# Kernel optimization log

Hardware: AMD Instinct MI355X
Metric: run time of the kernel (lower is better)

The kernel has to match this reference:

```python
import jax, jax.numpy as jnp
import numpy as np

QMAX = 127.0  # int8 symmetric
EPS = 1e-8

def _quant_dequant(v, axis):
    # symmetric int8 fake-quant along `axis` (per-row for weights, per-token for acts)
    scale = jnp.max(jnp.abs(v), axis=axis, keepdims=True) / QMAX
    scale = jnp.maximum(scale, EPS)
    q = jnp.clip(jnp.round(v / scale), -QMAX, QMAX)
    return q * scale

def _ste(v, axis):
    # straight-through estimator: identity gradient through quantization
    return v + jax.lax.stop_gradient(_quant_dequant(v, axis) - v)

def setup_inputs() -> dict:
    key = jax.random.key(0)
    k1, k2, k3 = jax.random.split(key, 3)
    H, I = 2048, 5632
    x = jax.random.normal(k1, (4, 2048, H), dtype=jnp.float32)
    # nn.Linear weight layout: [out_features, in_features]
    w_gate_up = jax.random.normal(k2, (2 * I, H), dtype=jnp.float32) * (H ** -0.5)
    w_down = jax.random.normal(k3, (H, I), dtype=jnp.float32) * (I ** -0.5)
    return {"x": x, "w_gate_up": w_gate_up, "w_down": w_down}

def reference(x, w_gate_up, w_down):
    I = w_down.shape[1]
    # QLinear #1: quantize act per-token, weight per-out-channel, dequant matmul
    xq = _ste(x, axis=-1)                       # [B,S,H]
    w1q = _ste(w_gate_up, axis=-1)              # [2I,H]
    gate_up = jnp.einsum('bsh,oh->bso', xq, w1q)  # [B,S,2I]
    gate, up = gate_up[..., :I], gate_up[..., I:]
    h = jax.nn.silu(gate) * up                  # SwiGLU, [B,S,I]
    # QLinear #2
    hq = _ste(h, axis=-1)
    w2q = _ste(w_down, axis=-1)                 # [H,I]
    return jnp.einsum('bsi,oi->bso', hq, w2q)   # [B,S,H]
```

## Files before the change

kernel.cpp:

```cpp
#include <hip/hip_runtime.h>
#include <hip/hip_bf16.h>
#include <stdint.h>

#define H_DIM 2048
#define I_DIM 5632
#define M_DIM 8192
#define N1_DIM (2 * I_DIM)
#define NBN1 (I_DIM / 128)
#define NPART (NBN1 * 4)
#define QS1 2304
#define QS2 5888

typedef __attribute__((ext_vector_type(4))) int i32x4;

__device__ __forceinline__ void gload16(const void* g, void* l) {
  __builtin_amdgcn_global_load_lds(
      reinterpret_cast<const __attribute__((address_space(1))) uint32_t*>(
          reinterpret_cast<uintptr_t>(g)),
      reinterpret_cast<__attribute__((address_space(3))) uint32_t*>(
          reinterpret_cast<uintptr_t>(l)),
      16, 0, 0);
}

__device__ __forceinline__ i32x4 ds_read128(uint32_t addr) {
  i32x4 d;
  asm volatile("s_mov_b32 m0, -1\n\tds_read_b128 %0, %1"
               : "=v"(d)
               : "v"(addr));
  return d;
}

#define MEMF() asm volatile("" ::: "memory")
#define BAR()                      \
  do {                             \
    MEMF();                        \
    __builtin_amdgcn_s_barrier();  \
    MEMF();                        \
  } while (0)
#define SCHEDB() __builtin_amdgcn_sched_barrier(0)

__global__ __launch_bounds__(256) void quant_rows_f32(
    const float* __restrict__ in, int8_t* __restrict__ q,
    float* __restrict__ scl, int rowlen, int qstride) {
  const int row = blockIdx.x;
  const int tid = threadIdx.x;
  const float* rp = in + (size_t)row * rowlen;
  float m = 0.f;
  for (int i = tid * 4; i < rowlen; i += 1024) {
    const float4 v = *reinterpret_cast<const float4*>(rp + i);
    m = fmaxf(m, fmaxf(fmaxf(fabsf(v.x), fabsf(v.y)),
                       fmaxf(fabsf(v.z), fabsf(v.w))));
  }
#pragma unroll
  for (int o = 32; o; o >>= 1) m = fmaxf(m, __shfl_xor(m, o));
  __shared__ float wm[4];
  if ((tid & 63) == 0) wm[tid >> 6] = m;
  __syncthreads();
  m = fmaxf(fmaxf(wm[0], wm[1]), fmaxf(wm[2], wm[3]));
  const float scale = fmaxf(m / 127.0f, 1e-8f);
  const float inv = 1.0f / scale;
  if (tid == 0) scl[row] = scale;
  int8_t* qp = q + (size_t)row * qstride;
  for (int i = tid * 4; i < rowlen; i += 1024) {
    const float4 v = *reinterpret_cast<const float4*>(rp + i);
    const int a = (int)rintf(fminf(fmaxf(v.x * inv, -127.f), 127.f));
    const int b = (int)rintf(fminf(fmaxf(v.y * inv, -127.f), 127.f));
    const int c = (int)rintf(fminf(fmaxf(v.z * inv, -127.f), 127.f));
    const int d = (int)rintf(fminf(fmaxf(v.w * inv, -127.f), 127.f));
    *reinterpret_cast<int*>(qp + i) =
        (a & 255) | ((b & 255) << 8) | ((c & 255) << 16) | (d << 24);
  }
}

__global__ __launch_bounds__(256) void quant_h_rows(
    const __hip_bfloat16* __restrict__ h, const float* __restrict__ hpart,
    int8_t* __restrict__ q, float* __restrict__ scl) {
  const int row = blockIdx.x;
  const int tid = threadIdx.x;
  float m = (tid < NPART) ? hpart[(size_t)row * NPART + tid] : 0.f;
#pragma unroll
  for (int o = 32; o; o >>= 1) m = fmaxf(m, __shfl_xor(m, o));
  __shared__ float wm[4];
  if ((tid & 63) == 0) wm[tid >> 6] = m;
  __syncthreads();
  m = fmaxf(fmaxf(wm[0], wm[1]), fmaxf(wm[2], wm[3]));
  const float scale = fmaxf(m / 127.0f, 1e-8f);
  const float inv = 1.0f / scale;
  if (tid == 0) scl[row] = scale;
  const __hip_bfloat16* rp = h + (size_t)row * I_DIM;
  int8_t* qp = q + (size_t)row * QS2;
  for (int i = tid * 8; i < I_DIM; i += 2048) {
    const uint4 v = *reinterpret_cast<const uint4*>(rp + i);
    const uint32_t w[4] = {v.x, v.y, v.z, v.w};
    int pk0 = 0, pk1 = 0;
#pragma unroll
    for (int j = 0; j < 8; ++j) {
      const float f =
          __uint_as_float(((w[j >> 1] >> ((j & 1) * 16)) & 0xffffu) << 16);
      const int qv = (int)rintf(fminf(fmaxf(f * inv, -127.f), 127.f));
      if (j < 4) pk0 |= (qv & 255) << ((j & 3) * 8);
      else       pk1 |= (qv & 255) << ((j & 3) * 8);
    }
    *reinterpret_cast<int2*>(qp + i) = make_int2(pk0, pk1);
  }
}

#define RD_A(MH, BUF)                                                          \
  do {                                                                         \
    _Pragma("unroll") for (int m = 0; m < 4; ++m) {                            \
      a[MH][m][0] = ds_read128(aB0 + (BUF) + (MH)*16384 + m * 2048);           \
      a[MH][m][1] = ds_read128(aB1 + (BUF) + (MH)*16384 + m * 2048);           \
    }                                                                          \
  } while (0)

#define RD_B(NH, BUF)                                                          \
  do {                                                                         \
    _Pragma("unroll") for (int n = 0; n < 2; ++n) {                            \
      b[NH][n][0] = ds_read128(bB0 + (BUF) + (NH)*16384 + n * 2048);           \
      b[NH][n][1] = ds_read128(bB1 + (BUF) + (NH)*16384 + n * 2048);           \
    }                                                                          \
  } while (0)

#define MFMA_Q(MH, NH)                                                         \
  do {                                                                         \
    __builtin_amdgcn_s_setprio(1);                                             \
    _Pragma("unroll") for (int kk = 0; kk < 2; ++kk)                           \
        _Pragma("unroll") for (int m = 0; m < 4; ++m)                          \
            _Pragma("unroll") for (int n = 0; n < 2; ++n) acc[MH][m][NH][n] =  \
        __builtin_amdgcn_mfma_i32_16x16x64_i8(a[MH][m][kk], b[NH][n][kk],      \
                                              acc[MH][m][NH][n], 0, 0, 0);     \
    __builtin_amdgcn_s_setprio(0);                                             \
  } while (0)

#define KTILE_BODY(SA, SB)                                                     \
  do {                                                                         \
    const int cb = (t & 1) * 32768;                                            \
    const int nb = cb ^ 32768;                                                 \
                                                                      \
    SCHEDB();                                                                  \
    RD_B(1, cb);                                                               \
    MEMF();                                                                    \
    if (t + 1 < KT) SA(1, t + 1);                                              \
    asm volatile("s_waitcnt lgkmcnt(4)" ::: "memory");                         \
    SCHEDB();                                                                  \
    MFMA_Q(0, 0);                                                              \
    BAR();                                                                     \
                                                                      \
    SCHEDB();                                                                  \
    RD_A(1, cb);                                                               \
    MEMF();                                                                    \
    if (t + 1 < KT) SB(1, t + 1);                                              \
    asm volatile("s_waitcnt lgkmcnt(8)" ::: "memory");                         \
    SCHEDB();                                                                  \
    MFMA_Q(0, 1);                                                              \
    BAR();                                                                     \
                                                                      \
    SCHEDB();                                                                  \
    if (t + 2 < KT) SA(0, t + 2);                                              \
    asm volatile("s_waitcnt lgkmcnt(0)" ::: "memory");                         \
    SCHEDB();                                                                  \
    MFMA_Q(1, 0);                                                              \
    if (t + 2 < KT) asm volatile("s_waitcnt vmcnt(6)" ::: "memory");           \
    else            asm volatile("s_waitcnt vmcnt(0)" ::: "memory");           \
    BAR();                                                                     \
                                                                      \
    SCHEDB();                                                                  \
    if (t + 1 < KT) { RD_A(0, nb); RD_B(0, nb); }                              \
    MEMF();                                                                    \
    if (t + 2 < KT) SB(0, t + 2);                                              \
    MFMA_Q(1, 1);                                                              \
    if (t + 1 < KT) {                                                          \
      if (t + 2 < KT) asm volatile("s_waitcnt vmcnt(4)" ::: "memory");         \
      else            asm volatile("s_waitcnt vmcnt(0)" ::: "memory");         \
    }                                                                          \
    BAR();                                                                     \
  } while (0)

__global__ __launch_bounds__(512, 2) void gemm1_silu(
    const int8_t* __restrict__ qx, const float* __restrict__ sx,
    const int8_t* __restrict__ qw, const float* __restrict__ sw,
    __hip_bfloat16* __restrict__ h, float* __restrict__ hpart) {
  __shared__ int8_t lds[131072];
  const int tid = threadIdx.x;
  const int lane = tid & 63;
  const int wid = tid >> 6;
  const int wr = wid >> 2, wc = wid & 3;
  const int c16 = lane & 15, kq = lane >> 4, r7 = lane & 7, lr = lane >> 3;
  const int sslot = ((lane & 7) ^ lr) << 4;
  const int sl0 = (kq ^ r7) << 4;
  const int sl1 = ((4 + kq) ^ r7) << 4;

  const int id = blockIdx.x;
  const int x = id & 7;
  const int j = id >> 3;
  const int bm = ((x & 1) << 4) + j / 11;
  const int bn = (x >> 1) * 11 + j % 11;

  const int xrow = wid * 8 + lr;
  const int fx = (xrow & ~31) | ((xrow & 15) << 1) | ((xrow >> 4) & 1);

  const size_t goffA = (size_t)(bm * 256 + xrow) * QS1 + sslot;
  const size_t goffG = (size_t)(bn * 128 + fx) * QS1 + sslot;
  const size_t goffU = goffG + (size_t)I_DIM * QS1;
  const int ldsAw = wid * 8 * 128;
  const int ldsBw = 65536 + wid * 8 * 128;

  const uint32_t L = (uint32_t)(uintptr_t)(void*)&lds[0];
  const uint32_t aB0 = L + (wr * 64 + c16) * 128 + sl0;
  const uint32_t aB1 = L + (wr * 64 + c16) * 128 + sl1;
  const uint32_t bB0 = L + 65536 + (wc * 32 + c16) * 128 + sl0;
  const uint32_t bB1 = L + 65536 + (wc * 32 + c16) * 128 + sl1;

  i32x4 acc[2][4][2][2] = {};
  i32x4 a[2][4][2], b[2][2][2];

#define STAGE_A1(half, t)                                                      \
  do {                                                                         \
    const int _b = ((t) & 1) * 32768;                                          \
    _Pragma("unroll") for (int ld = 0; ld < 2; ++ld)                           \
        gload16(qx + goffA + (size_t)((half)*128 + ld * 64) * QS1 +            \
                    (size_t)(t) * 128,                                         \
                lds + _b + ldsAw + ((half)*128 + ld * 64) * 128);              \
  } while (0)

#define STAGE_B1(half, t)                                                      \
  do {                                                                         \
    const int _b = ((t) & 1) * 32768;                                          \
    const int8_t* _s = (half) ? (qw + goffU) : (qw + goffG);                   \
    _Pragma("unroll") for (int ld = 0; ld < 2; ++ld)                           \
        gload16(_s + (size_t)(ld * 64) * QS1 + (size_t)(t) * 128,              \
                lds + _b + ldsBw + ((half)*128 + ld * 64) * 128);              \
  } while (0)

  const int KT = H_DIM / 128;
  STAGE_A1(0, 0); STAGE_B1(0, 0); STAGE_A1(1, 0); STAGE_B1(1, 0);
  STAGE_A1(0, 1); STAGE_B1(0, 1);
  asm volatile("s_waitcnt vmcnt(4)" ::: "memory");
  BAR();
  RD_A(0, 0); RD_B(0, 0);
  MEMF();

#pragma unroll 1
  for (int t = 0; t < KT; ++t) {
    KTILE_BODY(STAGE_A1, STAGE_B1);
  }

  const int row0 = bm * 256 + wr * 64 + kq * 4;
  const int colb = bn * 128 + wc * 32 + 2 * c16;
#pragma unroll
  for (int mh = 0; mh < 2; ++mh) {
#pragma unroll
    for (int m = 0; m < 4; ++m) {
#pragma unroll
      for (int r = 0; r < 4; ++r) {
        const int row = row0 + mh * 128 + m * 16 + r;
        const float sxr = sx[row];
        float hv[2];
#pragma unroll
        for (int n = 0; n < 2; ++n) {
          const int col = colb + n;
          const float g = (float)acc[mh][m][0][n][r] * (sxr * sw[col]);
          const float u = (float)acc[mh][m][1][n][r] * (sxr * sw[I_DIM + col]);
          hv[n] = g / (1.f + __expf(-g)) * u;
        }
        const uint32_t p0 = __bfloat16_as_ushort(__float2bfloat16(hv[0]));
        const uint32_t p1 = __bfloat16_as_ushort(__float2bfloat16(hv[1]));
        *reinterpret_cast<uint32_t*>(&h[(size_t)row * I_DIM + colb]) =
            p0 | (p1 << 16);
        float rmax = fmaxf(fabsf(hv[0]), fabsf(hv[1]));
#pragma unroll
        for (int o = 1; o < 16; o <<= 1)
          rmax = fmaxf(rmax, __shfl_xor(rmax, o));
        if (c16 == 0)
          hpart[(size_t)row * NPART + bn * 4 + wc] = rmax;
      }
    }
  }
}

__global__ __launch_bounds__(512, 2) void gemm2(
    const int8_t* __restrict__ qh, const float* __restrict__ sh,
    const int8_t* __restrict__ qw, const float* __restrict__ sw,
    float* __restrict__ out) {
  __shared__ int8_t lds[131072];
  const int tid = threadIdx.x;
  const int lane = tid & 63;
  const int wid = tid >> 6;
  const int wr = wid >> 2, wc = wid & 3;
  const int c16 = lane & 15, kq = lane >> 4, r7 = lane & 7, lr = lane >> 3;
  const int sslot = ((lane & 7) ^ lr) << 4;
  const int sl0 = (kq ^ r7) << 4;
  const int sl1 = ((4 + kq) ^ r7) << 4;

  const int nwg = gridDim.x;
  const int id = blockIdx.x;
  const int swz = (id & 7) * (nwg >> 3) + (id >> 3);
  const int NBN = H_DIM / 256;
  const int bm = swz / NBN, bn = swz % NBN;

  const size_t goffA = (size_t)(bm * 256 + wid * 8 + lr) * QS2 + sslot;
  const size_t goffB = (size_t)(bn * 256 + wid * 8 + lr) * QS2 + sslot;
  const int ldsAw = wid * 8 * 128;
  const int ldsBw = 65536 + wid * 8 * 128;

  const uint32_t L = (uint32_t)(uintptr_t)(void*)&lds[0];
  const uint32_t aB0 = L + (wr * 64 + c16) * 128 + sl0;
  const uint32_t aB1 = L + (wr * 64 + c16) * 128 + sl1;
  const uint32_t bB0 = L + 65536 + (wc * 32 + c16) * 128 + sl0;
  const uint32_t bB1 = L + 65536 + (wc * 32 + c16) * 128 + sl1;

  i32x4 acc[2][4][2][2] = {};
  i32x4 a[2][4][2], b[2][2][2];

#define STAGE_A2(half, t)                                                      \
  do {                                                                         \
    const int _b = ((t) & 1) * 32768;                                          \
    _Pragma("unroll") for (int ld = 0; ld < 2; ++ld)                           \
        gload16(qh + goffA + (size_t)((half)*128 + ld * 64) * QS2 +            \
                    (size_t)(t) * 128,                                         \
                lds + _b + ldsAw + ((half)*128 + ld * 64) * 128);              \
  } while (0)

#define STAGE_B2(half, t)                                                      \
  do {                                                                         \
    const int _b = ((t) & 1) * 32768;                                          \
    _Pragma("unroll") for (int ld = 0; ld < 2; ++ld)                           \
        gload16(qw + goffB + (size_t)((half)*128 + ld * 64) * QS2 +            \
                    (size_t)(t) * 128,                                         \
                lds + _b + ldsBw + ((half)*128 + ld * 64) * 128);              \
  } while (0)

  const int KT = I_DIM / 128;
  STAGE_A2(0, 0); STAGE_B2(0, 0); STAGE_A2(1, 0); STAGE_B2(1, 0);
  STAGE_A2(0, 1); STAGE_B2(0, 1);
  asm volatile("s_waitcnt vmcnt(4)" ::: "memory");
  BAR();
  RD_A(0, 0); RD_B(0, 0);
  MEMF();

#pragma unroll 1
  for (int t = 0; t < KT; ++t) {
    KTILE_BODY(STAGE_A2, STAGE_B2);
  }

  const int row0 = bm * 256 + wr * 64 + kq * 4;
  const int col0 = bn * 256 + wc * 32 + c16;
#pragma unroll
  for (int mh = 0; mh < 2; ++mh) {
#pragma unroll
    for (int m = 0; m < 4; ++m) {
#pragma unroll
      for (int r = 0; r < 4; ++r) {
        const int row = row0 + mh * 128 + m * 16 + r;
        const float shr = sh[row];
#pragma unroll
        for (int nh = 0; nh < 2; ++nh) {
#pragma unroll
          for (int n = 0; n < 2; ++n) {
            const int col = col0 + nh * 128 + n * 16;
            out[(size_t)row * H_DIM + col] =
                (float)acc[mh][m][nh][n][r] * (shr * sw[col]);
          }
        }
      }
    }
  }
}

extern "C" void kernel_launch(void* const* d_in, const int* in_sizes, int n_in,
                              void* d_out, int out_size, void* d_ws, size_t ws_size,
                              hipStream_t stream) {
  (void)in_sizes; (void)n_in; (void)out_size; (void)ws_size;
  const float* x  = (const float*)d_in[0];
  const float* w1 = (const float*)d_in[1];
  const float* w2 = (const float*)d_in[2];
  float* out = (float*)d_out;

  size_t off = 0;
  auto alloc = [&](size_t n) {
    void* p = (char*)d_ws + off;
    off += (n + 255) & ~(size_t)255;
    return p;
  };
  int8_t* qx  = (int8_t*)alloc((size_t)M_DIM * QS1);
  int8_t* qw1 = (int8_t*)alloc((size_t)N1_DIM * QS1);
  int8_t* qw2 = (int8_t*)alloc((size_t)H_DIM * QS2);
  int8_t* qh  = (int8_t*)alloc((size_t)M_DIM * QS2);
  __hip_bfloat16* hb = (__hip_bfloat16*)alloc((size_t)M_DIM * I_DIM * 2);
  float* sx    = (float*)alloc((size_t)M_DIM * 4);
  float* sw1   = (float*)alloc((size_t)N1_DIM * 4);
  float* sw2   = (float*)alloc((size_t)H_DIM * 4);
  float* shs   = (float*)alloc((size_t)M_DIM * 4);
  float* hpart = (float*)alloc((size_t)M_DIM * NPART * 4);

  quant_rows_f32<<<M_DIM, 256, 0, stream>>>(x, qx, sx, H_DIM, QS1);
  quant_rows_f32<<<N1_DIM, 256, 0, stream>>>(w1, qw1, sw1, H_DIM, QS1);
  quant_rows_f32<<<H_DIM, 256, 0, stream>>>(w2, qw2, sw2, I_DIM, QS2);
  gemm1_silu<<<(M_DIM / 256) * NBN1, 512, 0, stream>>>(
      qx, sx, qw1, sw1, hb, hpart);
  quant_h_rows<<<M_DIM, 256, 0, stream>>>(hb, hpart, qh, shs);
  gemm2<<<(M_DIM / 256) * (H_DIM / 256), 512, 0, stream>>>(
      qh, shs, qw2, sw2, out);
}
```

Before: 399.1 us.

## Halve GEMM K-tile to 64 and shrink LDS footprint to 64KB

Both int8 GEMM kernels move from a 128-wide K tile to a 64-wide one. This halves the double-buffered LDS allocation to 64KB and reworks the staging layout, the swizzle and the waitcnt counts to match. The smaller footprint is meant to let more workgroups stay resident per CU or to ease LDS pressure. In exchange the loop runs twice as many iterations with half as much MFMA work per barrier, so synchronisation overhead per FLOP goes up.

```diff
diff --git a/kernel.cpp b/kernel.cpp
--- a/kernel.cpp
+++ b/kernel.cpp
@@ -105,72 +105,67 @@
   }
 }
 
-#define RD_A(MH, BUF)                                                          \
+#define RD64_A(MH, BUF)                                                        \
   do {                                                                         \
-    _Pragma("unroll") for (int m = 0; m < 4; ++m) {                            \
-      a[MH][m][0] = ds_read128(aB0 + (BUF) + (MH)*16384 + m * 2048);           \
-      a[MH][m][1] = ds_read128(aB1 + (BUF) + (MH)*16384 + m * 2048);           \
-    }                                                                          \
-  } while (0)
-
-#define RD_B(NH, BUF)                                                          \
+    _Pragma("unroll") for (int m = 0; m < 4; ++m)                              \
+        a[MH][m] = ds_read128(aB + (BUF) + (MH)*8192 + m * 1024);              \
+  } while (0)
+
+#define RD64_B(NH, BUF)                                                        \
   do {                                                                         \
-    _Pragma("unroll") for (int n = 0; n < 2; ++n) {                            \
-      b[NH][n][0] = ds_read128(bB0 + (BUF) + (NH)*16384 + n * 2048);           \
-      b[NH][n][1] = ds_read128(bB1 + (BUF) + (NH)*16384 + n * 2048);           \
-    }                                                                          \
-  } while (0)
-
-#define MFMA_Q(MH, NH)                                                         \
+    _Pragma("unroll") for (int n = 0; n < 2; ++n)                              \
+        b[NH][n] = ds_read128(bB + (BUF) + (NH)*8192 + n * 1024);              \
+  } while (0)
+
+#define MFMA64_Q(MH, NH)                                                       \
   do {                                                                         \
     __builtin_amdgcn_s_setprio(1);                                             \
-    _Pragma("unroll") for (int kk = 0; kk < 2; ++kk)                           \
-        _Pragma("unroll") for (int m = 0; m < 4; ++m)                          \
-            _Pragma("unroll") for (int n = 0; n < 2; ++n) acc[MH][m][NH][n] =  \
-        __builtin_amdgcn_mfma_i32_16x16x64_i8(a[MH][m][kk], b[NH][n][kk],      \
+    _Pragma("unroll") for (int m = 0; m < 4; ++m)                              \
+        _Pragma("unroll") for (int n = 0; n < 2; ++n) acc[MH][m][NH][n] =      \
+        __builtin_amdgcn_mfma_i32_16x16x64_i8(a[MH][m], b[NH][n],              \
                                               acc[MH][m][NH][n], 0, 0, 0);     \
     __builtin_amdgcn_s_setprio(0);                                             \
   } while (0)
 
-#define KTILE_BODY(SA, SB)                                                     \
+#define KTILE64(SA, SB)                                                        \
   do {                                                                         \
-    const int cb = (t & 1) * 32768;                                            \
-    const int nb = cb ^ 32768;                                                 \
+    const int cb = (t & 1) * 16384;                                            \
+    const int nb = cb ^ 16384;                                                 \
                                                                       \
     SCHEDB();                                                                  \
-    RD_B(1, cb);                                                               \
+    RD64_B(1, cb);                                                             \
     MEMF();                                                                    \
     if (t + 1 < KT) SA(1, t + 1);                                              \
-    asm volatile("s_waitcnt lgkmcnt(4)" ::: "memory");                         \
-    SCHEDB();                                                                  \
-    MFMA_Q(0, 0);                                                              \
+    asm volatile("s_waitcnt lgkmcnt(2)" ::: "memory");                         \
+    SCHEDB();                                                                  \
+    MFMA64_Q(0, 0);                                                            \
     BAR();                                                                     \
                                                                       \
     SCHEDB();                                                                  \
-    RD_A(1, cb);                                                               \
+    RD64_A(1, cb);                                                             \
     MEMF();                                                                    \
     if (t + 1 < KT) SB(1, t + 1);                                              \
-    asm volatile("s_waitcnt lgkmcnt(8)" ::: "memory");                         \
-    SCHEDB();                                                                  \
-    MFMA_Q(0, 1);                                                              \
+    asm volatile("s_waitcnt lgkmcnt(4)" ::: "memory");                         \
+    SCHEDB();                                                                  \
+    MFMA64_Q(0, 1);                                                            \
     BAR();                                                                     \
                                                                       \
     SCHEDB();                                                                  \
     if (t + 2 < KT) SA(0, t + 2);                                              \
     asm volatile("s_waitcnt lgkmcnt(0)" ::: "memory");                         \
     SCHEDB();                                                                  \
-    MFMA_Q(1, 0);                                                              \
-    if (t + 2 < KT) asm volatile("s_waitcnt vmcnt(6)" ::: "memory");           \
+    MFMA64_Q(1, 0);                                                            \
+    if (t + 2 < KT) asm volatile("s_waitcnt vmcnt(3)" ::: "memory");           \
     else            asm volatile("s_waitcnt vmcnt(0)" ::: "memory");           \
     BAR();                                                                     \
                                                                       \
     SCHEDB();                                                                  \
-    if (t + 1 < KT) { RD_A(0, nb); RD_B(0, nb); }                              \
+    if (t + 1 < KT) { RD64_A(0, nb); RD64_B(0, nb); }                          \
     MEMF();                                                                    \
     if (t + 2 < KT) SB(0, t + 2);                                              \
-    MFMA_Q(1, 1);                                                              \
+    MFMA64_Q(1, 1);                                                            \
     if (t + 1 < KT) {                                                          \
-      if (t + 2 < KT) asm volatile("s_waitcnt vmcnt(4)" ::: "memory");         \
+      if (t + 2 < KT) asm volatile("s_waitcnt vmcnt(2)" ::: "memory");         \
       else            asm volatile("s_waitcnt vmcnt(0)" ::: "memory");         \
     }                                                                          \
     BAR();                                                                     \
@@ -180,15 +175,12 @@
     const int8_t* __restrict__ qx, const float* __restrict__ sx,
     const int8_t* __restrict__ qw, const float* __restrict__ sw,
     __hip_bfloat16* __restrict__ h, float* __restrict__ hpart) {
-  __shared__ int8_t lds[131072];
+  __shared__ int8_t lds[65536];
   const int tid = threadIdx.x;
   const int lane = tid & 63;
   const int wid = tid >> 6;
   const int wr = wid >> 2, wc = wid & 3;
-  const int c16 = lane & 15, kq = lane >> 4, r7 = lane & 7, lr = lane >> 3;
-  const int sslot = ((lane & 7) ^ lr) << 4;
-  const int sl0 = (kq ^ r7) << 4;
-  const int sl1 = ((4 + kq) ^ r7) << 4;
+  const int c16 = lane & 15, kq = lane >> 4;
 
   const int id = blockIdx.x;
   const int x = id & 7;
@@ -196,53 +188,42 @@
   const int bm = ((x & 1) << 4) + j / 11;
   const int bn = (x >> 1) * 11 + j % 11;
 
-  const int xrow = wid * 8 + lr;
-  const int fx = (xrow & ~31) | ((xrow & 15) << 1) | ((xrow >> 4) & 1);
-
-  const size_t goffA = (size_t)(bm * 256 + xrow) * QS1 + sslot;
+  const int srow = lane >> 2;
+  const int sslot = ((lane & 3) ^ (srow & 3)) << 4;
+  const int x0 = wid * 16 + srow;
+  const int fx = (x0 & ~31) | ((x0 & 15) << 1) | ((x0 >> 4) & 1);
+
+  const size_t goffA = (size_t)(bm * 256 + x0) * QS1 + sslot;
   const size_t goffG = (size_t)(bn * 128 + fx) * QS1 + sslot;
   const size_t goffU = goffG + (size_t)I_DIM * QS1;
-  const int ldsAw = wid * 8 * 128;
-  const int ldsBw = 65536 + wid * 8 * 128;
+  const int ldsW = wid * 1024;
 
   const uint32_t L = (uint32_t)(uintptr_t)(void*)&lds[0];
-  const uint32_t aB0 = L + (wr * 64 + c16) * 128 + sl0;
-  const uint32_t aB1 = L + (wr * 64 + c16) * 128 + sl1;
-  const uint32_t bB0 = L + 65536 + (wc * 32 + c16) * 128 + sl0;
-  const uint32_t bB1 = L + 65536 + (wc * 32 + c16) * 128 + sl1;
+  const uint32_t aB = L + (wr * 64 + c16) * 64 + ((kq ^ (c16 & 3)) << 4);
+  const uint32_t bB =
+      L + 32768 + (wc * 32 + c16) * 64 + ((kq ^ (c16 & 3)) << 4);
 
   i32x4 acc[2][4][2][2] = {};
-  i32x4 a[2][4][2], b[2][2][2];
-
-#define STAGE_A1(half, t)                                                      \
-  do {                                                                         \
-    const int _b = ((t) & 1) * 32768;                                          \
-    _Pragma("unroll") for (int ld = 0; ld < 2; ++ld)                           \
-        gload16(qx + goffA + (size_t)((half)*128 + ld * 64) * QS1 +            \
-                    (size_t)(t) * 128,                                         \
-                lds + _b + ldsAw + ((half)*128 + ld * 64) * 128);              \
-  } while (0)
-
-#define STAGE_B1(half, t)                                                      \
-  do {                                                                         \
-    const int _b = ((t) & 1) * 32768;                                          \
-    const int8_t* _s = (half) ? (qw + goffU) : (qw + goffG);                   \
-    _Pragma("unroll") for (int ld = 0; ld < 2; ++ld)                           \
-        gload16(_s + (size_t)(ld * 64) * QS1 + (size_t)(t) * 128,              \
-                lds + _b + ldsBw + ((half)*128 + ld * 64) * 128);              \
-  } while (0)
-
-  const int KT = H_DIM / 128;
-  STAGE_A1(0, 0); STAGE_B1(0, 0); STAGE_A1(1, 0); STAGE_B1(1, 0);
-  STAGE_A1(0, 1); STAGE_B1(0, 1);
-  asm volatile("s_waitcnt vmcnt(4)" ::: "memory");
+  i32x4 a[2][4], b[2][2];
+
+#define STG1A(half, t)                                                         \
+  gload16(qx + goffA + (size_t)(half) * 128 * QS1 + (size_t)(t) * 64,          \
+          lds + ((t) & 1) * 16384 + (half) * 8192 + ldsW)
+#define STG1B(half, t)                                                         \
+  gload16(((half) ? (qw + goffU) : (qw + goffG)) + (size_t)(t) * 64,           \
+          lds + 32768 + ((t) & 1) * 16384 + (half) * 8192 + ldsW)
+
+  const int KT = H_DIM / 64;
+  STG1A(0, 0); STG1B(0, 0); STG1A(1, 0); STG1B(1, 0);
+  STG1A(0, 1); STG1B(0, 1);
+  asm volatile("s_waitcnt vmcnt(2)" ::: "memory");
   BAR();
-  RD_A(0, 0); RD_B(0, 0);
+  RD64_A(0, 0); RD64_B(0, 0);
   MEMF();
 
 #pragma unroll 1
   for (int t = 0; t < KT; ++t) {
-    KTILE_BODY(STAGE_A1, STAGE_B1);
+    KTILE64(STG1A, STG1B);
   }
 
   const int row0 = bm * 256 + wr * 64 + kq * 4;
@@ -282,15 +263,12 @@
     const int8_t* __restrict__ qh, const float* __restrict__ sh,
     const int8_t* __restrict__ qw, const float* __restrict__ sw,
     float* __restrict__ out) {
-  __shared__ int8_t lds[131072];
+  __shared__ int8_t lds[65536];
   const int tid = threadIdx.x;
   const int lane = tid & 63;
   const int wid = tid >> 6;
   const int wr = wid >> 2, wc = wid & 3;
-  const int c16 = lane & 15, kq = lane >> 4, r7 = lane & 7, lr = lane >> 3;
-  const int sslot = ((lane & 7) ^ lr) << 4;
-  const int sl0 = (kq ^ r7) << 4;
-  const int sl1 = ((4 + kq) ^ r7) << 4;
+  const int c16 = lane & 15, kq = lane >> 4;
 
   const int nwg = gridDim.x;
   const int id = blockIdx.x;
@@ -298,49 +276,40 @@
   const int NBN = H_DIM / 256;
   const int bm = swz / NBN, bn = swz % NBN;
 
-  const size_t goffA = (size_t)(bm * 256 + wid * 8 + lr) * QS2 + sslot;
-  const size_t goffB = (size_t)(bn * 256 + wid * 8 + lr) * QS2 + sslot;
-  const int ldsAw = wid * 8 * 128;
-  const int ldsBw = 65536 + wid * 8 * 128;
+  const int srow = lane >> 2;
+  const int sslot = ((lane & 3) ^ (srow & 3)) << 4;
+  const int x0 = wid * 16 + srow;
+
+  const size_t goffA = (size_t)(bm * 256 + x0) * QS2 + sslot;
+  const size_t goffB = (size_t)(bn * 256 + x0) * QS2 + sslot;
+  const int ldsW = wid * 1024;
 
   const uint32_t L = (uint32_t)(uintptr_t)(void*)&lds[0];
-  const uint32_t aB0 = L + (wr * 64 + c16) * 128 + sl0;
-  const uint32_t aB1 = L + (wr * 64 + c16) * 128 + sl1;
-  const uint32_t bB0 = L + 65536 + (wc * 32 + c16) * 128 + sl0;
-  const uint32_t bB1 = L + 65536 + (wc * 32 + c16) * 128 + sl1;
+  const uint32_t aB = L + (wr * 64 + c16) * 64 + ((kq ^ (c16 & 3)) << 4);
+  const uint32_t bB =
+      L + 32768 + (wc * 32 + c16) * 64 + ((kq ^ (c16 & 3)) << 4);
 
   i32x4 acc[2][4][2][2] = {};
-  i32x4 a[2][4][2], b[2][2][2];
-
-#define STAGE_A2(half, t)                                                      \
-  do {                                                                         \
-    const int _b = ((t) & 1) * 32768;                                          \
-    _Pragma("unroll") for (int ld = 0; ld < 2; ++ld)                           \
-        gload16(qh + goffA + (size_t)((half)*128 + ld * 64) * QS2 +            \
-                    (size_t)(t) * 128,                                         \
-                lds + _b + ldsAw + ((half)*128 + ld * 64) * 128);              \
-  } while (0)
-
-#define STAGE_B2(half, t)                                                      \
-  do {                                                                         \
-    const int _b = ((t) & 1) * 32768;                                          \
-    _Pragma("unroll") for (int ld = 0; ld < 2; ++ld)                           \
-        gload16(qw + goffB + (size_t)((half)*128 + ld * 64) * QS2 +            \
-                    (size_t)(t) * 128,                                         \
-                lds + _b + ldsBw + ((half)*128 + ld * 64) * 128);              \
-  } while (0)
-
-  const int KT = I_DIM / 128;
-  STAGE_A2(0, 0); STAGE_B2(0, 0); STAGE_A2(1, 0); STAGE_B2(1, 0);
-  STAGE_A2(0, 1); STAGE_B2(0, 1);
-  asm volatile("s_waitcnt vmcnt(4)" ::: "memory");
+  i32x4 a[2][4], b[2][2];
+
+#define STG2A(half, t)                                                         \
+  gload16(qh + goffA + (size_t)(half) * 128 * QS2 + (size_t)(t) * 64,          \
+          lds + ((t) & 1) * 16384 + (half) * 8192 + ldsW)
+#define STG2B(half, t)                                                         \
+  gload16(qw + goffB + (size_t)(half) * 128 * QS2 + (size_t)(t) * 64,          \
+          lds + 32768 + ((t) & 1) * 16384 + (half) * 8192 + ldsW)
+
+  const int KT = I_DIM / 64;
+  STG2A(0, 0); STG2B(0, 0); STG2A(1, 0); STG2B(1, 0);
+  STG2A(0, 1); STG2B(0, 1);
+  asm volatile("s_waitcnt vmcnt(2)" ::: "memory");
   BAR();
-  RD_A(0, 0); RD_B(0, 0);
+  RD64_A(0, 0); RD64_B(0, 0);
   MEMF();
 
 #pragma unroll 1
   for (int t = 0; t < KT; ++t) {
-    KTILE_BODY(STAGE_A2, STAGE_B2);
+    KTILE64(STG2A, STG2B);
   }
 
   const int row0 = bm * 256 + wr * 64 + kq * 4;
```

Result: slower. 435.9 us (+9.2%).
